# Kernel tuning notes

Measured on AMD Instinct MI355X. Metric: run time of the kernel, lower is better.

The kernel has to match this reference:

```python
import jax, jax.numpy as jnp
import numpy as np

N_NODES = 100000
EMB = 256
HID = 64
N_REL = 5
N_EDGES = 3200000
BATCH = 16384


def _rgcn_conv(x, W, root, b, src, dst, etype):
    # PyG RGCNConv with mean aggregation per relation:
    # out_i = sum_r mean_{j in N_r(i)} x_j @ W_r + x_i @ root + b
    N = x.shape[0]
    R = W.shape[0]
    h = jnp.einsum('ni,rio->rno', x, W)          # [R, N, O] per-relation transforms
    m = h[etype, src]                            # [E, O] per-edge messages
    seg = dst * R + etype                        # combined (node, relation) segment id
    sums = jax.ops.segment_sum(m, seg, num_segments=N * R)
    cnt = jax.ops.segment_sum(jnp.ones((m.shape[0],), dtype=x.dtype), seg,
                              num_segments=N * R)
    mean = sums / jnp.maximum(cnt, 1.0)[:, None]
    agg = mean.reshape(N, R, -1).sum(axis=1)     # sum over relations
    return agg + x @ root + b


def _merge(x1, x2, w1, b1, w2, b2):
    x = jnp.concatenate([x1, x2], axis=1)
    h = jax.nn.relu(x @ w1 + b1)
    return h @ w2 + b2                           # [B, 1] logits


def setup_inputs() -> dict:
    key = jax.random.key(0)
    ks = jax.random.split(key, 16)
    d = {}
    d['bill_id'] = jax.random.randint(ks[0], (BATCH,), 0, N_NODES)
    d['user1_id'] = jax.random.randint(ks[1], (BATCH,), 0, N_NODES)
    d['user2_id'] = jax.random.randint(ks[2], (BATCH,), 0, N_NODES)
    d['edge_index'] = jax.random.randint(ks[3], (2, N_EDGES), 0, N_NODES)
    d['edge_type'] = jax.random.randint(ks[4], (N_EDGES,), 0, N_REL)
    # learned params (xavier-ish scaling); linear weights stored as [in, out]
    d['users_feature'] = jax.random.normal(ks[5], (N_NODES, EMB), jnp.float32) * 0.06
    d['W1'] = jax.random.normal(ks[6], (N_REL, EMB, HID), jnp.float32) * 0.08
    d['root1'] = jax.random.normal(ks[7], (EMB, HID), jnp.float32) * 0.08
    d['b1'] = jnp.zeros((HID,), jnp.float32)
    d['W2'] = jax.random.normal(ks[8], (N_REL, HID, HID), jnp.float32) * 0.12
    d['root2'] = jax.random.normal(ks[9], (HID, HID), jnp.float32) * 0.12
    d['b2'] = jnp.zeros((HID,), jnp.float32)
    d['mfc1_w'] = jax.random.normal(ks[10], (2 * HID, HID), jnp.float32) * 0.1
    d['mfc1_b'] = jnp.zeros((HID,), jnp.float32)
    d['mfc2_w'] = jax.random.normal(ks[11], (HID, 1), jnp.float32) * 0.17
    d['mfc2_b'] = jnp.zeros((1,), jnp.float32)
    return d


def reference(bill_id, user1_id, user2_id, edge_index, edge_type,
              users_feature, W1, root1, b1, W2, root2, b2,
              mfc1_w, mfc1_b, mfc2_w, mfc2_b):
    src, dst = edge_index[0], edge_index[1]
    x = jax.nn.relu(_rgcn_conv(users_feature, W1, root1, b1, src, dst, edge_type))
    nodes = _rgcn_conv(x, W2, root2, b2, src, dst, edge_type)  # [N, 64]
    bill = nodes[bill_id]
    u1 = nodes[user1_id]
    u2 = nodes[user2_id]
    pos = _merge(bill, u1, mfc1_w, mfc1_b, mfc2_w, mfc2_b)  # [B, 1]
    neg = _merge(bill, u2, mfc1_w, mfc1_b, mfc2_w, mfc2_b)
    z = jnp.concatenate([pos, neg], axis=0)
    t = jnp.concatenate([jnp.ones_like(pos), jnp.zeros_like(pos)], axis=0)
    # numerically stable BCE-with-logits, mean reduction
    bce = jnp.mean(jnp.maximum(z, 0.0) - z * t + jnp.log1p(jnp.exp(-jnp.abs(z))))
    pred = jnp.round(jax.nn.sigmoid(z))
    acc = jnp.mean((pred == t).astype(jnp.float32))
    return (bce, acc)
```

## Files before the change

### kernel.cpp

```cpp
#include <hip/hip_runtime.h>
#include <hip/hip_bf16.h>

#define N_NODES 100000
#define EMB 256
#define HID 64
#define N_REL 5
#define N_EDGES 3200000
#define BATCH 16384
#define NB 782
#define NWG1 256
#define CH 12500
#define LSEG 640
#define NSEG (N_NODES * N_REL)

typedef unsigned short u16;
typedef unsigned int u32;
typedef __attribute__((ext_vector_type(4))) float f32x4;
typedef __attribute__((ext_vector_type(8))) short short8;

__device__ __forceinline__ float bf2f(u16 u) {
    union { float f; u32 i; } v;
    v.i = ((u32)u) << 16;
    return v.f;
}
__device__ __forceinline__ u16 f2bf(float f) {
    union { float f; u32 i; } v;
    v.f = f;
    u32 r = v.i + 0x7fff + ((v.i >> 16) & 1);
    return (u16)(r >> 16);
}
__device__ __forceinline__ short8 pack8(float4 a, float4 b) {
    short8 r;
    r[0] = (short)f2bf(a.x); r[1] = (short)f2bf(a.y);
    r[2] = (short)f2bf(a.z); r[3] = (short)f2bf(a.w);
    r[4] = (short)f2bf(b.x); r[5] = (short)f2bf(b.y);
    r[6] = (short)f2bf(b.z); r[7] = (short)f2bf(b.w);
    return r;
}

__device__ __forceinline__ void gload_lds16(const void* g, void* l) {
    __builtin_amdgcn_global_load_lds(
        (const __attribute__((address_space(1))) unsigned int*)g,
        (__attribute__((address_space(3))) unsigned int*)l, 16, 0, 0);
}

__global__ __launch_bounds__(256) void bucket_hist(const int* __restrict__ dst,
                                                   int* __restrict__ hist) {
    __shared__ int hl[NB];
    const int tid = threadIdx.x;
    for (int i = tid; i < NB; i += 256) hl[i] = 0;
    __syncthreads();
    const int w = blockIdx.x;
    const int s = w * CH, e = s + CH;
    for (int i = s + tid; i < e; i += 256)
        atomicAdd(&hl[dst[i] >> 7], 1);
    __syncthreads();
    for (int i = tid; i < NB; i += 256) hist[w * NB + i] = hl[i];
}

__global__ void col_scan(int* __restrict__ hist, int* __restrict__ btot) {
    const int b = blockIdx.x;
    const int lane = threadIdx.x;
    int carry = 0;
    for (int c = 0; c < NWG1; c += 64) {
        int v = hist[(c + lane) * NB + b];
        int incl = v;
#pragma unroll
        for (int off = 1; off < 64; off <<= 1) {
            int t = __shfl_up(incl, off);
            if (lane >= off) incl += t;
        }
        hist[(c + lane) * NB + b] = carry + (incl - v);
        carry += __shfl(incl, 63);
    }
    if (lane == 0) btot[b] = carry;
}

__global__ void btot_scan(const int* __restrict__ btot, int* __restrict__ boffs,
                          int* __restrict__ offs) {
    const int lane = threadIdx.x;
    int carry = 0;
    for (int c = 0; c < NB; c += 64) {
        int v = (c + lane < NB) ? btot[c + lane] : 0;
        int incl = v;
#pragma unroll
        for (int off = 1; off < 64; off <<= 1) {
            int t = __shfl_up(incl, off);
            if (lane >= off) incl += t;
        }
        if (c + lane < NB) boffs[c + lane] = carry + (incl - v);
        carry += __shfl(incl, 63);
    }
    if (lane == 0) {
        boffs[NB] = N_EDGES;
        offs[NSEG] = N_EDGES;
    }
}

__global__ __launch_bounds__(256) void bucket_scatter(
        const int* __restrict__ src, const int* __restrict__ dst,
        const int* __restrict__ et, const int* __restrict__ base,
        const int* __restrict__ boffs, u32* __restrict__ bucketed) {
    __shared__ int cur[NB];
    const int tid = threadIdx.x;
    const int w = blockIdx.x;
    for (int i = tid; i < NB; i += 256) cur[i] = boffs[i] + base[w * NB + i];
    __syncthreads();
    const int s = w * CH, e = s + CH;
    for (int i = s + tid; i < e; i += 256) {
        int d = dst[i];
        int b = d >> 7;
        u32 key = (u32)src[i] | ((u32)((d & 127) * 5 + et[i]) << 17);
        int pos = atomicAdd(&cur[b], 1);
        bucketed[pos] = key;
    }
}

__global__ __launch_bounds__(256) void seg_sort(
        const u32* __restrict__ keys, const int* __restrict__ boffs,
        int* __restrict__ offs, u32* __restrict__ soff) {
    __shared__ int cntl[LSEG];
    __shared__ int cur[LSEG];
    const int tid = threadIdx.x;
    const int b = blockIdx.x;
    const int s = boffs[b], e = boffs[b + 1];

    for (int i = tid; i < LSEG; i += 256) cntl[i] = 0;
    __syncthreads();
    for (int i = s + tid; i < e; i += 256)
        atomicAdd(&cntl[keys[i] >> 17], 1);
    __syncthreads();

    if (tid < 64) {
        int carry = 0;
        for (int c = 0; c < LSEG; c += 64) {
            int v = cntl[c + tid];
            int incl = v;
#pragma unroll
            for (int off = 1; off < 64; off <<= 1) {
                int t = __shfl_up(incl, off);
                if (tid >= off) incl += t;
            }
            cur[c + tid] = carry + (incl - v);
            carry += __shfl(incl, 63);
        }
    }
    __syncthreads();

    const int segbase = b * LSEG;
    for (int i = tid; i < LSEG; i += 256)
        if (segbase + i < NSEG) offs[segbase + i] = s + cur[i];
    __syncthreads();

    for (int i = s + tid; i < e; i += 256) {
        u32 key = keys[i];
        u32 lseg = key >> 17;
        int pos = s + atomicAdd(&cur[lseg], 1);
        u32 q = (lseg * 52429u) >> 18;
        u32 rel = lseg - q * 5u;
        soff[pos] = (key & 0x1FFFF) * 384u + rel * 64u;
    }
}

__global__ void build_bt(const float* __restrict__ W, const float* __restrict__ root,
                         int K, u16* __restrict__ BT) {
    int idx = blockIdx.x * blockDim.x + threadIdx.x;
    if (idx >= 384 * K) return;
    int j = idx / K, k = idx - j * K;
    float v = (j < 320) ? W[((j >> 6) * K + k) * 64 + (j & 63)]
                        : root[k * 64 + (j & 63)];
    BT[idx] = f2bf(v);
}

template <int K, bool A_F32>
__global__ __launch_bounds__(512) void gemm384(
        const void* __restrict__ Av, const u16* __restrict__ BT,
        u16* __restrict__ C) {
    __shared__ __align__(16) u16 Al[128 * 64];
    __shared__ __align__(16) u16 Bl[384 * 64];
    const int tid  = threadIdx.x;
    const int lane = tid & 63;
    const int w    = tid >> 6;
    const int m0 = blockIdx.x * 128;
    const int wr = (w >> 2) * 64;
    const int wc = (w & 3) * 96;
    const int l15 = lane & 15;
    const int lg  = lane >> 4;

    f32x4 acc[4][6];
#pragma unroll
    for (int i = 0; i < 4; ++i)
#pragma unroll
        for (int j = 0; j < 6; ++j) {
            f32x4 z = {0.f, 0.f, 0.f, 0.f};
            acc[i][j] = z;
        }

    for (int k0 = 0; k0 < K; k0 += 64) {
#pragma unroll
        for (int j = 0; j < 6; ++j) {
            int c = (j * 8 + w) * 64 + lane;
            int row = c >> 3, sub = c & 7;
            gload_lds16(BT + (size_t)row * K + k0 + ((sub ^ (row & 7)) * 8),
                        &Bl[(j * 8 + w) * 512]);
        }
        if (A_F32) {
            const float* Af = (const float*)Av;
            int row = tid >> 2;
            int q0  = (tid & 3) * 2;
            int grow = min(m0 + row, N_NODES - 1);
            const float4* p = (const float4*)(Af + (size_t)grow * K + k0 + q0 * 8);
            float4 v0 = p[0], v1 = p[1], v2 = p[2], v3 = p[3];
            *(short8*)&Al[row * 64 + ((q0 ^ (row & 7)) * 8)]       = pack8(v0, v1);
            *(short8*)&Al[row * 64 + (((q0 + 1) ^ (row & 7)) * 8)] = pack8(v2, v3);
        } else {
            const u16* Ab = (const u16*)Av;
#pragma unroll
            for (int i = 0; i < 2; ++i) {
                int c = (i * 8 + w) * 64 + lane;
                int row = c >> 3, sub = c & 7;
                gload_lds16(Ab + (size_t)(m0 + row) * K + k0 + ((sub ^ (row & 7)) * 8),
                            &Al[(i * 8 + w) * 512]);
            }
        }
        __syncthreads();

#pragma unroll
        for (int kk = 0; kk < 64; kk += 32) {
            const int ch = (kk >> 3) + lg;
            short8 af[4], bf[6];
#pragma unroll
            for (int f = 0; f < 4; ++f) {
                int row = wr + f * 16 + l15;
                af[f] = *(const short8*)&Al[row * 64 + ((ch ^ (row & 7)) * 8)];
            }
#pragma unroll
            for (int f = 0; f < 6; ++f) {
                int col = wc + f * 16 + l15;
                bf[f] = *(const short8*)&Bl[col * 64 + ((ch ^ (col & 7)) * 8)];
            }
#pragma unroll
            for (int fm = 0; fm < 4; ++fm)
#pragma unroll
                for (int fn = 0; fn < 6; ++fn)
                    acc[fm][fn] = __builtin_amdgcn_mfma_f32_16x16x32_bf16(
                        bf[fn], af[fm], acc[fm][fn], 0, 0, 0);
        }
        __syncthreads();
    }

    char* Cst = (char*)Bl;
#pragma unroll
    for (int half = 0; half < 2; ++half) {
        if ((w >> 2) == half) {
#pragma unroll
            for (int fm = 0; fm < 4; ++fm) {
                int row_l = fm * 16 + l15;
#pragma unroll
                for (int fn = 0; fn < 6; ++fn) {
                    ushort4 p;
                    p.x = f2bf(acc[fm][fn][0]); p.y = f2bf(acc[fm][fn][1]);
                    p.z = f2bf(acc[fm][fn][2]); p.w = f2bf(acc[fm][fn][3]);
                    int colb  = (wc + fn * 16 + lg * 4) * 2;
                    int chunk = colb >> 4;
                    int addr  = row_l * 768 + (((chunk ^ (row_l & 7)) << 4) | (colb & 15));
                    *(ushort4*)(Cst + addr) = p;
                }
            }
        }
        __syncthreads();
#pragma unroll
        for (int it = 0; it < 6; ++it) {
            int idx = it * 512 + tid;
            int row_l = idx / 48;
            int chk = idx - row_l * 48;
            int r = m0 + half * 64 + row_l;
            if (r < N_NODES) {
                float4 v = *(const float4*)(Cst + row_l * 768 + ((chk ^ (row_l & 7)) << 4));
                *(float4*)(C + (size_t)r * 384 + chk * 8) = v;
            }
        }
        __syncthreads();
    }
}

template <bool RELU>
__global__ __launch_bounds__(256) void agg_rl(
        const u16* __restrict__ h, const u32* __restrict__ soff,
        const int* __restrict__ offs, const float* __restrict__ bias,
        u16* __restrict__ out) {
    const int lane = threadIdx.x & 63;
    const int d = (blockIdx.x * blockDim.x + threadIdx.x) >> 6;
    if (d >= N_NODES) return;

    const int o0 = offs[d * 5 + 0], o1 = offs[d * 5 + 1], o2 = offs[d * 5 + 2];
    const int o3 = offs[d * 5 + 3], o4 = offs[d * 5 + 4], o5 = offs[d * 5 + 5];
    const float i0 = 1.f / (float)max(o1 - o0, 1);
    const float i1 = 1.f / (float)max(o2 - o1, 1);
    const float i2 = 1.f / (float)max(o3 - o2, 1);
    const float i3 = 1.f / (float)max(o4 - o3, 1);
    const float i4 = 1.f / (float)max(o5 - o4, 1);

    const u16* hl = h + lane;
    float acc0 = bf2f(h[(size_t)d * 384 + 320 + lane]) + bias[lane];
    float acc1 = 0.f;

    for (int base = o0; base < o5; base += 64) {
        const int idx = base + lane;
        const u32 voff = soff[min(idx, o5 - 1)];
        float wv = idx < o1 ? i0 : idx < o2 ? i1 : idx < o3 ? i2
                 : idx < o4 ? i3 : i4;
        if (idx >= o5) wv = 0.f;
        const int m = min(64, o5 - base);
        for (int j = 0; j < m; j += 8) {
#pragma unroll
            for (int jj = 0; jj < 8; jj += 2) {
                int  offa = __builtin_amdgcn_readlane((int)voff, j + jj);
                int  wa_i = __builtin_amdgcn_readlane((int)__float_as_uint(wv), j + jj);
                int  offb = __builtin_amdgcn_readlane((int)voff, j + jj + 1);
                int  wb_i = __builtin_amdgcn_readlane((int)__float_as_uint(wv), j + jj + 1);
                acc0 += bf2f(hl[(u32)offa]) * __uint_as_float((u32)wa_i);
                acc1 += bf2f(hl[(u32)offb]) * __uint_as_float((u32)wb_i);
            }
        }
    }
    float acc = acc0 + acc1;
    if (RELU) acc = fmaxf(acc, 0.f);
    out[(size_t)d * 64 + lane] = f2bf(acc);
}

__global__ __launch_bounds__(256) void loss_kernel(
        const u16* __restrict__ nodes, const int* __restrict__ bill,
        const int* __restrict__ u1, const int* __restrict__ u2,
        const float* __restrict__ w1, const float* __restrict__ b1,
        const float* __restrict__ w2, const float* __restrict__ b2,
        float* __restrict__ out) {
    __shared__ float Wl[128 * 64];
    __shared__ float red[2][4];
    for (int j = threadIdx.x; j < 128 * 16; j += 256)
        ((float4*)Wl)[j] = ((const float4*)w1)[j];
    __syncthreads();

    const int lane = threadIdx.x & 63;
    const int wv   = threadIdx.x >> 6;
    const int gw   = blockIdx.x * 4 + wv;
    const int nw   = gridDim.x * 4;

    const float bias1 = b1[lane];
    const float w2l   = w2[lane];
    const float bias2 = b2[0];

    float bce_acc = 0.f, corr_acc = 0.f;
    for (int s = gw; s < BATCH; s += nw) {
        const u16* xb  = nodes + (size_t)bill[s] * 64;
        const u16* xu1 = nodes + (size_t)u1[s] * 64;
        const u16* xu2 = nodes + (size_t)u2[s] * 64;
        float hb = bias1, h1 = 0.f, h2 = 0.f;
#pragma unroll 8
        for (int i = 0; i < 64; ++i) {
            float wb = Wl[i * 64 + lane];
            float wu = Wl[(64 + i) * 64 + lane];
            hb += bf2f(xb[i]) * wb;
            h1 += bf2f(xu1[i]) * wu;
            h2 += bf2f(xu2[i]) * wu;
        }
        float p1 = fmaxf(hb + h1, 0.f) * w2l;
        float p2 = fmaxf(hb + h2, 0.f) * w2l;
#pragma unroll
        for (int off = 32; off > 0; off >>= 1) {
            p1 += __shfl_down(p1, off);
            p2 += __shfl_down(p2, off);
        }
        if (lane == 0) {
            float z1 = p1 + bias2;
            float z2 = p2 + bias2;
            bce_acc += fmaxf(z1, 0.f) - z1 + log1pf(expf(-fabsf(z1)));
            bce_acc += fmaxf(z2, 0.f)      + log1pf(expf(-fabsf(z2)));
            corr_acc += (z1 > 0.f) ? 1.f : 0.f;
            corr_acc += (z2 > 0.f) ? 0.f : 1.f;
        }
    }
    if (lane == 0) { red[0][wv] = bce_acc; red[1][wv] = corr_acc; }
    __syncthreads();
    if (threadIdx.x == 0) {
        const float scale = 1.f / (2.f * BATCH);
        atomicAdd(&out[0], (red[0][0] + red[0][1] + red[0][2] + red[0][3]) * scale);
        atomicAdd(&out[1], (red[1][0] + red[1][1] + red[1][2] + red[1][3]) * scale);
    }
}

extern "C" void kernel_launch(void* const* d_in, const int* in_sizes, int n_in,
                              void* d_out, int out_size, void* d_ws, size_t ws_size,
                              hipStream_t stream) {
    const int*   bill  = (const int*)d_in[0];
    const int*   u1    = (const int*)d_in[1];
    const int*   u2    = (const int*)d_in[2];
    const int*   ei    = (const int*)d_in[3];
    const int*   et    = (const int*)d_in[4];
    const float* uf    = (const float*)d_in[5];
    const float* W1    = (const float*)d_in[6];
    const float* root1 = (const float*)d_in[7];
    const float* b1    = (const float*)d_in[8];
    const float* W2    = (const float*)d_in[9];
    const float* root2 = (const float*)d_in[10];
    const float* b2    = (const float*)d_in[11];
    const float* m1w   = (const float*)d_in[12];
    const float* m1b   = (const float*)d_in[13];
    const float* m2w   = (const float*)d_in[14];
    const float* m2b   = (const float*)d_in[15];
    float* out = (float*)d_out;

    char* ws = (char*)d_ws;
    u16* h_all    = (u16*)(ws);
    u32* sorted   = (u32*)(ws + 76800000);
    u32* bucketed = (u32*)(ws + 89600000);
    u16* xbuf     = (u16*)(ws + 89600000);
    int* hist     = (int*)(ws + 102400000);
    int* btot     = (int*)(ws + 103200768);
    int* boffs    = (int*)(ws + 103203896);
    int* offs     = (int*)(ws + 103207040);
    u16* BT1      = (u16*)(ws + 105207056);
    u16* BT2      = (u16*)(ws + 105403664);
    if (ws_size < 105452816) return;

    const int* src = ei;
    const int* dst = ei + N_EDGES;

    hipMemsetAsync(d_out, 0, 2 * sizeof(float), stream);

    bucket_hist<<<NWG1, 256, 0, stream>>>(dst, hist);
    col_scan<<<NB, 64, 0, stream>>>(hist, btot);
    btot_scan<<<1, 64, 0, stream>>>(btot, boffs, offs);
    bucket_scatter<<<NWG1, 256, 0, stream>>>(src, dst, et, hist, boffs, bucketed);
    seg_sort<<<NB, 256, 0, stream>>>(bucketed, boffs, offs, sorted);

    build_bt<<<(384 * EMB + 255) / 256, 256, 0, stream>>>(W1, root1, EMB, BT1);
    build_bt<<<(384 * HID + 255) / 256, 256, 0, stream>>>(W2, root2, HID, BT2);

    gemm384<EMB, true><<<782, 512, 0, stream>>>(uf, BT1, h_all);
    agg_rl<true><<<25000, 256, 0, stream>>>(h_all, sorted, offs, b1, xbuf);

    gemm384<HID, false><<<782, 512, 0, stream>>>(xbuf, BT2, h_all);
    agg_rl<false><<<25000, 256, 0, stream>>>(h_all, sorted, offs, b2, xbuf);

    loss_kernel<<<1024, 256, 0, stream>>>(xbuf, bill, u1, u2, m1w, m1b, m2w, m2b, out);
}
```

Baseline: 364.7 us.

## Aggregate-then-transform for second RGCN layer in fused gather+MFMA kernel

The second layer now averages the 64-wide layer-1 features per relation first and only then multiplies by the stacked W2/root2 matrix. This is done in a new fused kernel that gathers 16 nodes into LDS and runs a bf16 MFMA. It replaces the 384-wide h_all gemm plus its gather, which cuts gathered bytes per edge and drops a kernel launch and the BT2 build. The sorted edge array now stores plain source ids, and the relation offset is rebuilt inside agg_rl. The trade-off is an extra bf16 rounding of the means and a serial per-relation loop in each wave with weaker memory-level parallelism.

```diff
diff --git a/kernel.cpp b/kernel.cpp
--- a/kernel.cpp
+++ b/kernel.cpp
@@ -12,6 +12,7 @@
 #define CH 12500
 #define LSEG 640
 #define NSEG (N_NODES * N_REL)
+#define NGRP 6250
 
 typedef unsigned short u16;
 typedef unsigned int u32;
@@ -118,7 +119,7 @@
 
 __global__ __launch_bounds__(256) void seg_sort(
         const u32* __restrict__ keys, const int* __restrict__ boffs,
-        int* __restrict__ offs, u32* __restrict__ soff) {
+        int* __restrict__ offs, u32* __restrict__ ssrc) {
     __shared__ int cntl[LSEG];
     __shared__ int cur[LSEG];
     const int tid = threadIdx.x;
@@ -154,11 +155,8 @@
 
     for (int i = s + tid; i < e; i += 256) {
         u32 key = keys[i];
-        u32 lseg = key >> 17;
-        int pos = s + atomicAdd(&cur[lseg], 1);
-        u32 q = (lseg * 52429u) >> 18;
-        u32 rel = lseg - q * 5u;
-        soff[pos] = (key & 0x1FFFF) * 384u + rel * 64u;
+        int pos = s + atomicAdd(&cur[key >> 17], 1);
+        ssrc[pos] = key & 0x1FFFF;
     }
 }
 
@@ -286,7 +284,7 @@
 
 template <bool RELU>
 __global__ __launch_bounds__(256) void agg_rl(
-        const u16* __restrict__ h, const u32* __restrict__ soff,
+        const u16* __restrict__ h, const u32* __restrict__ ssrc,
         const int* __restrict__ offs, const float* __restrict__ bias,
         u16* __restrict__ out) {
     const int lane = threadIdx.x & 63;
@@ -307,10 +305,16 @@
 
     for (int base = o0; base < o5; base += 64) {
         const int idx = base + lane;
-        const u32 voff = soff[min(idx, o5 - 1)];
-        float wv = idx < o1 ? i0 : idx < o2 ? i1 : idx < o3 ? i2
-                 : idx < o4 ? i3 : i4;
+        const u32 s = ssrc[min(idx, o5 - 1)];
+        u32 reladd;
+        float wv;
+        if (idx < o1)      { reladd = 0;   wv = i0; }
+        else if (idx < o2) { reladd = 64;  wv = i1; }
+        else if (idx < o3) { reladd = 128; wv = i2; }
+        else if (idx < o4) { reladd = 192; wv = i3; }
+        else               { reladd = 256; wv = i4; }
         if (idx >= o5) wv = 0.f;
+        const u32 voff = s * 384u + reladd;
         const int m = min(64, o5 - base);
         for (int j = 0; j < m; j += 8) {
 #pragma unroll
@@ -327,6 +331,75 @@
     float acc = acc0 + acc1;
     if (RELU) acc = fmaxf(acc, 0.f);
     out[(size_t)d * 64 + lane] = f2bf(acc);
+}
+
+__global__ __launch_bounds__(1024) void agg_mm(
+        const u16* __restrict__ x1, const u32* __restrict__ ssrc,
+        const int* __restrict__ offs, const float* __restrict__ W2,
+        const float* __restrict__ root2, const float* __restrict__ b2,
+        u16* __restrict__ outn) {
+    __shared__ __align__(16) u16 WT[64 * 392];
+    __shared__ __align__(16) u16 Al[16 * 392];
+    const int tid  = threadIdx.x;
+    const int lane = tid & 63;
+    const int wv   = tid >> 6;
+    const int l15  = lane & 15;
+    const int lg   = lane >> 4;
+
+    for (int i = tid; i < 384 * 64; i += 1024) {
+        int j = i >> 6, o = i & 63;
+        float v = (j < 320) ? W2[i] : root2[i - 320 * 64];
+        WT[o * 392 + j] = f2bf(v);
+    }
+    __syncthreads();
+
+    const float b2v = b2[(wv & 3) * 16 + l15];
+
+    for (int g = blockIdx.x; g < NGRP; g += gridDim.x) {
+        const int n = g * 16 + wv;
+        int o[6];
+#pragma unroll
+        for (int r = 0; r < 6; ++r) o[r] = offs[n * 5 + r];
+        Al[wv * 392 + 320 + lane] = x1[(size_t)n * 64 + lane];
+#pragma unroll
+        for (int rel = 0; rel < 5; ++rel) {
+            const int os = o[rel], oe = o[rel + 1];
+            float macc = 0.f;
+            if (oe > os) {
+                for (int base = os; base < oe; base += 64) {
+                    u32 off = ssrc[min(base + lane, oe - 1)] << 6;
+                    const int m = min(64, oe - base);
+                    for (int j = 0; j < m; j += 8) {
+#pragma unroll
+                        for (int jj = 0; jj < 8; ++jj) {
+                            if (j + jj < m) {
+                                int ov = __builtin_amdgcn_readlane((int)off, j + jj);
+                                macc += bf2f(x1[(u32)ov + lane]);
+                            }
+                        }
+                    }
+                }
+                macc *= 1.f / (float)(oe - os);
+            }
+            Al[wv * 392 + rel * 64 + lane] = f2bf(macc);
+        }
+        __syncthreads();
+        if (wv < 4) {
+            f32x4 acc = {0.f, 0.f, 0.f, 0.f};
+#pragma unroll
+            for (int ks = 0; ks < 12; ++ks) {
+                short8 af = *(const short8*)&Al[l15 * 392 + ks * 32 + lg * 8];
+                short8 bf = *(const short8*)&WT[(wv * 16 + l15) * 392 + ks * 32 + lg * 8];
+                acc = __builtin_amdgcn_mfma_f32_16x16x32_bf16(af, bf, acc, 0, 0, 0);
+            }
+            const int n0 = g * 16;
+#pragma unroll
+            for (int i = 0; i < 4; ++i)
+                outn[(size_t)(n0 + lg * 4 + i) * 64 + wv * 16 + l15] =
+                    f2bf(acc[i] + b2v);
+        }
+        __syncthreads();
+    }
 }
 
 __global__ __launch_bounds__(256) void loss_kernel(
@@ -412,7 +485,7 @@
 
     char* ws = (char*)d_ws;
     u16* h_all    = (u16*)(ws);
-    u32* sorted   = (u32*)(ws + 76800000);
+    u32* ssrc     = (u32*)(ws + 76800000);
     u32* bucketed = (u32*)(ws + 89600000);
     u16* xbuf     = (u16*)(ws + 89600000);
     int* hist     = (int*)(ws + 102400000);
@@ -420,7 +493,6 @@
     int* boffs    = (int*)(ws + 103203896);
     int* offs     = (int*)(ws + 103207040);
     u16* BT1      = (u16*)(ws + 105207056);
-    u16* BT2      = (u16*)(ws + 105403664);
     if (ws_size < 105452816) return;
 
     const int* src = ei;
@@ -432,16 +504,14 @@
     col_scan<<<NB, 64, 0, stream>>>(hist, btot);
     btot_scan<<<1, 64, 0, stream>>>(btot, boffs, offs);
     bucket_scatter<<<NWG1, 256, 0, stream>>>(src, dst, et, hist, boffs, bucketed);
-    seg_sort<<<NB, 256, 0, stream>>>(bucketed, boffs, offs, sorted);
+    seg_sort<<<NB, 256, 0, stream>>>(bucketed, boffs, offs, ssrc);
 
     build_bt<<<(384 * EMB + 255) / 256, 256, 0, stream>>>(W1, root1, EMB, BT1);
-    build_bt<<<(384 * HID + 255) / 256, 256, 0, stream>>>(W2, root2, HID, BT2);
 
     gemm384<EMB, true><<<782, 512, 0, stream>>>(uf, BT1, h_all);
-    agg_rl<true><<<25000, 256, 0, stream>>>(h_all, sorted, offs, b1, xbuf);
-
-    gemm384<HID, false><<<782, 512, 0, stream>>>(xbuf, BT2, h_all);
-    agg_rl<false><<<25000, 256, 0, stream>>>(h_all, sorted, offs, b2, xbuf);
-
-    loss_kernel<<<1024, 256, 0, stream>>>(xbuf, bill, u1, u2, m1w, m1b, m2w, m2b, out);
-}
+    agg_rl<true><<<25000, 256, 0, stream>>>(h_all, ssrc, offs, b1, xbuf);
+
+    agg_mm<<<1024, 1024, 0, stream>>>(xbuf, ssrc, offs, W2, root2, b2, h_all);
+
+    loss_kernel<<<1024, 256, 0, stream>>>(h_all, bill, u1, u2, m1w, m1b, m2w, m2b, out);
+}
```

Measured after the change: 503.4 us. +38.0%, slower.
